# Performance work log

Measured on AMD Instinct MI355X. Metric: run time of the kernel, lower is better.

## Reference

```python
import jax, jax.numpy as jnp
import numpy as np

B, C = 32, 2048

def setup_inputs() -> dict:
    key = jax.random.key(0)
    k1, k2, k3 = jax.random.split(key, 3)
    x1 = jax.random.normal(k1, (B, C), dtype=jnp.float32)
    x2 = jax.random.normal(k2, (B, C), dtype=jnp.float32)
    # 1x1 conv over 2C->C channels on a 1x1 spatial map == dense layer (C, 2C)
    W = jax.random.normal(k3, (C, 2 * C), dtype=jnp.float32) * (1.0 / np.sqrt(2 * C))
    b = jnp.zeros((C,), dtype=jnp.float32)
    return {"x1": x1, "x2": x2, "W": W, "b": b}


def reference(x1, x2, W, b):
    # conv1x1 fusion of the two (B,C) inputs -> (B,C)
    x = jnp.concatenate([x1, x2], axis=1) @ W.T + b  # (B, C)
    # energy[b,i,j] = x[b,i] * x[b,j]  (H*W == 1 -> rank-1 outer product)
    energy = x[:, :, None] * x[:, None, :]  # (B, C, C)
    # max-subtraction variant: softmax(max_j(energy) - energy) along last dim
    energy_new = jnp.max(energy, axis=-1, keepdims=True) - energy
    attention = jax.nn.softmax(energy_new, axis=-1)  # (B, C, C)
    # attention @ value (value is (B,C,1) since H=W=1) -> matvec, then residual
    out1 = jnp.einsum('bij,bj->bi', attention, x1) + x1  # (B, C)
    out2 = jnp.einsum('bij,bj->bi', attention, x2) + x2  # (B, C)
    return out1, out2, attention
```

## Files before the change

kernel.cpp:

```cpp
#include <hip/hip_runtime.h>

#define CDIM 2048
#define BATCH 32
#define K2 4096

typedef float f32x4 __attribute__((ext_vector_type(4)));

#define BN 64
#define BK 128
#define KT (K2 / BK)
#define NT (CDIM / BN)

__global__ __launch_bounds__(256) void gemm_partial_k(
    const float* __restrict__ x1, const float* __restrict__ x2,
    const float* __restrict__ W, float* __restrict__ partial)
{
    __shared__ float Xs[BATCH][BK + 1];
    __shared__ float Wt[BN][BK + 1];
    const int nt = blockIdx.x, kt = blockIdx.y;
    const int i0 = nt * BN, k0 = kt * BK;
    const int t = threadIdx.x;

    const float* xsrc = (k0 < CDIM) ? x1 : x2;
    const int kk0 = k0 & (CDIM - 1);

    #pragma unroll
    for (int r = 0; r < 4; ++r) {
        int f = t + 256 * r;
        int b = f >> 5, c4 = (f & 31) * 4;
        float4 v = *reinterpret_cast<const float4*>(xsrc + b * CDIM + kk0 + c4);
        Xs[b][c4 + 0] = v.x; Xs[b][c4 + 1] = v.y;
        Xs[b][c4 + 2] = v.z; Xs[b][c4 + 3] = v.w;
    }
    #pragma unroll
    for (int r = 0; r < 8; ++r) {
        int f = t + 256 * r;
        int row = f >> 5, c4 = (f & 31) * 4;
        float4 v = *reinterpret_cast<const float4*>(W + (size_t)(i0 + row) * K2 + k0 + c4);
        Wt[row][c4 + 0] = v.x; Wt[row][c4 + 1] = v.y;
        Wt[row][c4 + 2] = v.z; Wt[row][c4 + 3] = v.w;
    }
    __syncthreads();

    const int j = t & 31, bg = t >> 5;
    const int il = j * 2, b0 = bg * 4;
    float acc[4][2] = {};
    #pragma unroll 4
    for (int kk = 0; kk < BK; ++kk) {
        float w0 = Wt[il][kk], w1 = Wt[il + 1][kk];
        #pragma unroll
        for (int bb = 0; bb < 4; ++bb) {
            float xv = Xs[b0 + bb][kk];
            acc[bb][0] = fmaf(xv, w0, acc[bb][0]);
            acc[bb][1] = fmaf(xv, w1, acc[bb][1]);
        }
    }
    #pragma unroll
    for (int bb = 0; bb < 4; ++bb) {
        float2 v = make_float2(acc[bb][0], acc[bb][1]);
        *reinterpret_cast<float2*>(partial + (size_t)kt * (BATCH * CDIM)
                                   + (b0 + bb) * CDIM + i0 + il) = v;
    }
}

__global__ __launch_bounds__(256) void reduce_x_k(
    const float* __restrict__ partial, const float* __restrict__ bias,
    float* __restrict__ x)
{
    int idx = blockIdx.x * 256 + threadIdx.x;
    float s = 0.f;
    #pragma unroll
    for (int kt = 0; kt < KT; ++kt) s += partial[(size_t)kt * (BATCH * CDIM) + idx];
    x[idx] = s + bias[idx & (CDIM - 1)];
}

__global__ __launch_bounds__(256) void attn_k(
    const float* __restrict__ x, const float* __restrict__ x1,
    const float* __restrict__ x2, float* __restrict__ out1,
    float* __restrict__ out2, float* __restrict__ att)
{
    __shared__ float xs[CDIM];
    __shared__ float wred[8];
    const int b = blockIdx.x >> 5, rg = blockIdx.x & 31;
    const int t = threadIdx.x;
    const int lane = t & 63, wv = t >> 6;
    const float* xb  = x  + b * CDIM;
    const float* x1b = x1 + b * CDIM;
    const float* x2b = x2 + b * CDIM;

    #pragma unroll
    for (int r = 0; r < 2; ++r) {
        int f = t + 256 * r;
        float4 v = *reinterpret_cast<const float4*>(xb + f * 4);
        *reinterpret_cast<float4*>(&xs[f * 4]) = v;
    }
    __syncthreads();

    float mn = 1e30f, mx = -1e30f;
    for (int f = t; f < CDIM; f += 256) {
        float v = xs[f];
        mn = fminf(mn, v); mx = fmaxf(mx, v);
    }
    #pragma unroll
    for (int off = 32; off > 0; off >>= 1) {
        mn = fminf(mn, __shfl_xor(mn, off));
        mx = fmaxf(mx, __shfl_xor(mx, off));
    }
    if (lane == 0) { wred[wv] = mn; wred[4 + wv] = mx; }
    __syncthreads();
    mn = fminf(fminf(wred[0], wred[1]), fminf(wred[2], wred[3]));
    mx = fmaxf(fmaxf(wred[4], wred[5]), fmaxf(wred[6], wred[7]));

    float x1r[8][4], x2r[8][4];
    #pragma unroll
    for (int g = 0; g < 8; ++g) {
        int o = g * 256 + lane * 4;
        float4 a = *reinterpret_cast<const float4*>(x1b + o);
        float4 c = *reinterpret_cast<const float4*>(x2b + o);
        x1r[g][0] = a.x; x1r[g][1] = a.y; x1r[g][2] = a.z; x1r[g][3] = a.w;
        x2r[g][0] = c.x; x2r[g][1] = c.y; x2r[g][2] = c.z; x2r[g][3] = c.w;
    }

    for (int r = 0; r < 16; ++r) {
        const int i = rg * 64 + wv * 16 + r;
        const float xi = xs[i];
        const float li = (xi >= 0.f) ? xi * mn : xi * mx;
        const float nxi = -xi;
        float e[8][4];
        float sum = 0.f, d1 = 0.f, d2 = 0.f;
        #pragma unroll
        for (int g = 0; g < 8; ++g) {
            float4 xv = *reinterpret_cast<const float4*>(&xs[g * 256 + lane * 4]);
            float xj[4] = {xv.x, xv.y, xv.z, xv.w};
            #pragma unroll
            for (int c = 0; c < 4; ++c) {
                float ev = __expf(fmaf(nxi, xj[c], li));
                e[g][c] = ev;
                sum += ev;
                d1 = fmaf(ev, x1r[g][c], d1);
                d2 = fmaf(ev, x2r[g][c], d2);
            }
        }
        #pragma unroll
        for (int off = 32; off > 0; off >>= 1) {
            sum += __shfl_xor(sum, off);
            d1  += __shfl_xor(d1, off);
            d2  += __shfl_xor(d2, off);
        }
        const float inv = 1.f / sum;
        if (lane == 0) {
            out1[b * CDIM + i] = fmaf(d1, inv, x1b[i]);
            out2[b * CDIM + i] = fmaf(d2, inv, x2b[i]);
        }
        float* arow = att + (size_t)(b * CDIM + i) * CDIM;
        #pragma unroll
        for (int g = 0; g < 8; ++g) {
            f32x4 v = { e[g][0] * inv, e[g][1] * inv, e[g][2] * inv, e[g][3] * inv };
            __builtin_nontemporal_store(v, reinterpret_cast<f32x4*>(arow + g * 256 + lane * 4));
        }
    }
}

extern "C" void kernel_launch(void* const* d_in, const int* in_sizes, int n_in,
                              void* d_out, int out_size, void* d_ws, size_t ws_size,
                              hipStream_t stream) {
    const float* x1   = (const float*)d_in[0];
    const float* x2   = (const float*)d_in[1];
    const float* W    = (const float*)d_in[2];
    const float* bias = (const float*)d_in[3];
    float* out  = (float*)d_out;
    float* out1 = out;
    float* out2 = out + BATCH * CDIM;
    float* att  = out + 2 * BATCH * CDIM;
    float* x    = (float*)d_ws;

    float* partial = out + ((size_t)out_size - (size_t)KT * BATCH * CDIM);

    gemm_partial_k<<<dim3(NT, KT), dim3(256), 0, stream>>>(x1, x2, W, partial);
    reduce_x_k<<<(BATCH * CDIM) / 256, 256, 0, stream>>>(partial, bias, x);
    attn_k<<<BATCH * (CDIM / 64), 256, 0, stream>>>(x, x1, x2, out1, out2, att);
}
```

Measured before the change: 133.0 us.

## Stage x1/x2 in shared memory, raise attn occupancy, drop nontemporal stores

The attention kernel now copies x1 and x2 into shared memory and reads them from there in the inner loop, where it used to keep 64 floats of them in registers. It also adds a minimum-blocks-per-SM launch bound of 4, so the lower register use can translate into higher occupancy. The attention output is now written with ordinary stores instead of nontemporal stores. The trade is extra LDS traffic in the inner loop and possibly worse cache behaviour for the large streaming write.

Result: slower. 191.2 us (+43.8%).

```diff
diff --git a/kernel.cpp b/kernel.cpp
--- a/kernel.cpp
+++ b/kernel.cpp
@@ -74,12 +74,14 @@
     x[idx] = s + bias[idx & (CDIM - 1)];
 }
 
-__global__ __launch_bounds__(256) void attn_k(
+__global__ __launch_bounds__(256, 4) void attn_k(
     const float* __restrict__ x, const float* __restrict__ x1,
     const float* __restrict__ x2, float* __restrict__ out1,
     float* __restrict__ out2, float* __restrict__ att)
 {
     __shared__ float xs[CDIM];
+    __shared__ float xs1[CDIM];
+    __shared__ float xs2[CDIM];
     __shared__ float wred[8];
     const int b = blockIdx.x >> 5, rg = blockIdx.x & 31;
     const int t = threadIdx.x;
@@ -90,9 +92,10 @@
 
     #pragma unroll
     for (int r = 0; r < 2; ++r) {
-        int f = t + 256 * r;
-        float4 v = *reinterpret_cast<const float4*>(xb + f * 4);
-        *reinterpret_cast<float4*>(&xs[f * 4]) = v;
+        int f = (t + 256 * r) * 4;
+        *reinterpret_cast<float4*>(&xs[f])  = *reinterpret_cast<const float4*>(xb  + f);
+        *reinterpret_cast<float4*>(&xs1[f]) = *reinterpret_cast<const float4*>(x1b + f);
+        *reinterpret_cast<float4*>(&xs2[f]) = *reinterpret_cast<const float4*>(x2b + f);
     }
     __syncthreads();
 
@@ -111,34 +114,26 @@
     mn = fminf(fminf(wred[0], wred[1]), fminf(wred[2], wred[3]));
     mx = fmaxf(fmaxf(wred[4], wred[5]), fmaxf(wred[6], wred[7]));
 
-    float x1r[8][4], x2r[8][4];
-    #pragma unroll
-    for (int g = 0; g < 8; ++g) {
-        int o = g * 256 + lane * 4;
-        float4 a = *reinterpret_cast<const float4*>(x1b + o);
-        float4 c = *reinterpret_cast<const float4*>(x2b + o);
-        x1r[g][0] = a.x; x1r[g][1] = a.y; x1r[g][2] = a.z; x1r[g][3] = a.w;
-        x2r[g][0] = c.x; x2r[g][1] = c.y; x2r[g][2] = c.z; x2r[g][3] = c.w;
-    }
-
     for (int r = 0; r < 16; ++r) {
         const int i = rg * 64 + wv * 16 + r;
         const float xi = xs[i];
         const float li = (xi >= 0.f) ? xi * mn : xi * mx;
         const float nxi = -xi;
-        float e[8][4];
+        f32x4 e[8];
         float sum = 0.f, d1 = 0.f, d2 = 0.f;
         #pragma unroll
         for (int g = 0; g < 8; ++g) {
-            float4 xv = *reinterpret_cast<const float4*>(&xs[g * 256 + lane * 4]);
-            float xj[4] = {xv.x, xv.y, xv.z, xv.w};
+            const int o = g * 256 + lane * 4;
+            f32x4 xv  = *reinterpret_cast<const f32x4*>(&xs[o]);
+            f32x4 v1  = *reinterpret_cast<const f32x4*>(&xs1[o]);
+            f32x4 v2  = *reinterpret_cast<const f32x4*>(&xs2[o]);
             #pragma unroll
             for (int c = 0; c < 4; ++c) {
-                float ev = __expf(fmaf(nxi, xj[c], li));
+                float ev = __expf(fmaf(nxi, xv[c], li));
                 e[g][c] = ev;
                 sum += ev;
-                d1 = fmaf(ev, x1r[g][c], d1);
-                d2 = fmaf(ev, x2r[g][c], d2);
+                d1 = fmaf(ev, v1[c], d1);
+                d2 = fmaf(ev, v2[c], d2);
             }
         }
         #pragma unroll
@@ -149,14 +144,14 @@
         }
         const float inv = 1.f / sum;
         if (lane == 0) {
-            out1[b * CDIM + i] = fmaf(d1, inv, x1b[i]);
-            out2[b * CDIM + i] = fmaf(d2, inv, x2b[i]);
+            out1[b * CDIM + i] = fmaf(d1, inv, xs1[i]);
+            out2[b * CDIM + i] = fmaf(d2, inv, xs2[i]);
         }
         float* arow = att + (size_t)(b * CDIM + i) * CDIM;
         #pragma unroll
         for (int g = 0; g < 8; ++g) {
-            f32x4 v = { e[g][0] * inv, e[g][1] * inv, e[g][2] * inv, e[g][3] * inv };
-            __builtin_nontemporal_store(v, reinterpret_cast<f32x4*>(arow + g * 256 + lane * 4));
+            f32x4 v = e[g] * inv;
+            *reinterpret_cast<f32x4*>(arow + g * 256 + lane * 4) = v;
         }
     }
 }
```
